# Kernel optimization log

Measured on AMD Instinct MI355X. Metric: run time of the kernel, lower is better.

The kernel has to match this reference:

```python
import jax, jax.numpy as jnp
import numpy as np

D = 1024      # dim_input
H = 16        # n_heads
DH = 64       # dim_inner
S = 1024      # current_seq
M = 1024      # pre_seq (memory)
B = 2         # batch
SCALE = 1.0 / np.sqrt(DH)


def _rel_shift(x):
    # x: [S, J, B, H]; Transformer-XL relative shift
    s, j = x.shape[0], x.shape[1]
    zero = jnp.zeros((s, 1) + x.shape[2:], x.dtype)
    x = jnp.concatenate([zero, x], axis=1)            # [S, J+1, B, H]
    x = x.reshape((j + 1, s) + x.shape[2:])[1:]        # [J, S, B, H]
    return x.reshape((s, j) + x.shape[2:])             # [S, J, B, H]


def setup_inputs() -> dict:
    key = jax.random.key(0)
    ks = jax.random.split(key, 9)
    std = 1.0 / np.sqrt(D)
    return {
        "multi_head_input": jax.random.normal(ks[0], (S, B, D), jnp.float32),
        "position_emb": jax.random.normal(ks[1], (S + M, D), jnp.float32),
        "memory": jax.random.normal(ks[2], (M, B, D), jnp.float32),
        "u": jax.random.normal(ks[3], (H, DH), jnp.float32) * 0.02,
        "v": jax.random.normal(ks[4], (H, DH), jnp.float32) * 0.02,
        "W_kv": jax.random.normal(ks[5], (D, 2 * H * DH), jnp.float32) * std,
        "W_q": jax.random.normal(ks[6], (D, H * DH), jnp.float32) * std,
        "W_pos": jax.random.normal(ks[7], (D, H * DH), jnp.float32) * std,
        "W_out": jax.random.normal(ks[8], (H * DH, D), jnp.float32) * std,
    }


def reference(multi_head_input, position_emb, memory, u, v, W_kv, W_q, W_pos, W_out):
    s = multi_head_input.shape[0]
    m = memory.shape[0]
    b = multi_head_input.shape[1]
    x_mem = jnp.concatenate([memory, multi_head_input], axis=0)   # [M+S, B, D]
    kv = x_mem @ W_kv                                              # [M+S, B, 2*H*DH]
    k, val = jnp.split(kv, 2, axis=-1)
    k = k.reshape(m + s, b, H, DH)
    val = val.reshape(m + s, b, H, DH)
    q = (multi_head_input @ W_q).reshape(s, b, H, DH)              # [S, B, H, DH]

    # content term: (q + u) . k
    content = jnp.einsum('ibhd,jbhd->ijbh', q + u, k)              # [S, M+S, B, H]
    # position term: (q + v) . r, then rel_shift
    r = (position_emb @ W_pos).reshape(m + s, H, DH)               # [M+S, H, DH]
    pos = jnp.einsum('ibhd,jhd->ijbh', q + v, r)                   # [S, M+S, B, H]
    pos = _rel_shift(pos)

    attn = jax.nn.softmax((content + pos) * SCALE, axis=1)         # [S, M+S, B, H]
    out = jnp.einsum('ijbh,jbhd->ibhd', attn, val).reshape(s, b, H * DH)
    return out @ W_out                                             # [S, B, D]
```

## Files before the change

kernel.cpp:

```cpp
#include <hip/hip_runtime.h>
#include <hip/hip_bf16.h>
#include <hip/hip_fp16.h>
#include <math.h>

#define D    1024
#define H    16
#define DH   64
#define S    1024
#define M    1024
#define B    2
#define J    2048
#define SCALE 0.125f

typedef __attribute__((ext_vector_type(8))) short        bf16x8;
typedef __attribute__((ext_vector_type(4))) short        s16x4;
typedef __attribute__((ext_vector_type(8))) _Float16     h16x8;
typedef __attribute__((ext_vector_type(8))) unsigned short us8;
typedef __attribute__((ext_vector_type(4))) float        f32x4;

__device__ __forceinline__ short f2bs(float f) {
    __hip_bfloat16 t = __float2bfloat16(f);
    short r; __builtin_memcpy(&r, &t, 2); return r;
}
__device__ __forceinline__ unsigned short f2bf_fast(float f) {
    unsigned int u; __builtin_memcpy(&u, &f, 4);
    return (unsigned short)((u + 0x8000u) >> 16);
}

__device__ __forceinline__ void g2l16(const short* g, short* l) {
    __builtin_amdgcn_global_load_lds(
        (const __attribute__((address_space(1))) unsigned int*)g,
        (__attribute__((address_space(3))) unsigned int*)l, 16, 0, 0);
}

__global__ __launch_bounds__(256)
void prep(const float* __restrict__ mem, const float* __restrict__ x,
          const float* __restrict__ pemb,
          const float* __restrict__ Wkv, const float* __restrict__ Wq,
          const float* __restrict__ Wpos, const float* __restrict__ Wout,
          short* __restrict__ a_bf, short* __restrict__ p_bf,
          short* __restrict__ wkvt, short* __restrict__ wqt,
          short* __restrict__ wpt,  short* __restrict__ wot)
{
    __shared__ float t[64][65];
    int blk = blockIdx.x;
    const int tid = threadIdx.x;
    if (blk < 6144) {
        const int idx = (blk * 256 + tid) * 4;
        const int TWO_M = 2 * 1024 * 1024;
        float4 v; short* dst;
        if (idx < TWO_M)          { v = *(const float4*)(mem  + idx);           dst = a_bf + idx; }
        else if (idx < 2 * TWO_M) { v = *(const float4*)(x    + idx - TWO_M);   dst = a_bf + idx; }
        else                      { v = *(const float4*)(pemb + idx - 2*TWO_M); dst = p_bf + idx - 2*TWO_M; }
        s16x4 o = { f2bs(v.x), f2bs(v.y), f2bs(v.z), f2bs(v.w) };
        *(s16x4*)dst = o;
        return;
    }
    blk -= 6144;
    const float* src; short* dst; int N, t0;
    if (blk < 512)       { src = Wkv;  dst = wkvt; N = 2048; t0 = blk; }
    else if (blk < 768)  { src = Wq;   dst = wqt;  N = 1024; t0 = blk - 512; }
    else if (blk < 1024) { src = Wpos; dst = wpt;  N = 1024; t0 = blk - 768; }
    else                 { src = Wout; dst = wot;  N = 1024; t0 = blk - 1024; }
    const int ntn = N >> 6;
    const int k0 = (t0 / ntn) * 64, n0 = (t0 % ntn) * 64;
    #pragma unroll
    for (int e = tid; e < 4096; e += 256) {
        int r = e >> 6, c = e & 63;
        t[r][c] = src[(size_t)(k0 + r) * N + n0 + c];
    }
    __syncthreads();
    #pragma unroll
    for (int e = tid; e < 4096; e += 256) {
        int nr = e >> 6, kc = e & 63;
        dst[(size_t)(n0 + nr) * 1024 + k0 + kc] = f2bs(t[kc][nr]);
    }
}

__device__ __forceinline__ void gemm_core(const short* __restrict__ A,
                                          const short* __restrict__ Bt,
                                          short* As, short* Bs,
                                          int bm0, int bn0, int tid,
                                          f32x4 acc[4][4])
{
    const int w    = tid >> 6;
    const int wy   = w >> 1, wx = w & 1;
    const int lane = tid & 63;
    const int lm   = lane & 15;
    const int lq   = lane >> 4;

    for (int k0 = 0; k0 < 1024; k0 += 64) {
        const short* Ab = A  + (size_t)bm0 * 1024 + k0;
        const short* Bb = Bt + (size_t)bn0 * 1024 + k0;
        #pragma unroll
        for (int t = 0; t < 4; ++t) {
            int s = t * 256 + tid;
            int r = s >> 3, c = s & 7;
            int cg = c ^ (r & 7);
            g2l16(Ab + r * 1024 + cg * 8, As + s * 8);
            g2l16(Bb + r * 1024 + cg * 8, Bs + s * 8);
        }
        __syncthreads();
        #pragma unroll
        for (int kk = 0; kk < 2; ++kk) {
            bf16x8 af[4], bg[4];
            #pragma unroll
            for (int r4 = 0; r4 < 4; ++r4) {
                int ar = wy * 64 + r4 * 16 + lm;
                int kc = kk * 4 + lq;
                af[r4] = *(const bf16x8*)(As + ((ar << 3) + (kc ^ (ar & 7))) * 8);
            }
            #pragma unroll
            for (int c4 = 0; c4 < 4; ++c4) {
                int br = wx * 64 + c4 * 16 + lm;
                int kc = kk * 4 + lq;
                bg[c4] = *(const bf16x8*)(Bs + ((br << 3) + (kc ^ (br & 7))) * 8);
            }
            #pragma unroll
            for (int r4 = 0; r4 < 4; ++r4)
                #pragma unroll
                for (int c4 = 0; c4 < 4; ++c4)
                    acc[r4][c4] = __builtin_amdgcn_mfma_f32_16x16x32_bf16(
                        af[r4], bg[c4], acc[r4][c4], 0, 0, 0);
        }
        __syncthreads();
    }
}

__global__ __launch_bounds__(256)
void proj_fused(const short* __restrict__ a_bf, const short* __restrict__ p_bf,
                const short* __restrict__ wkvt, const short* __restrict__ wqt,
                const short* __restrict__ wpt,
                short* __restrict__ k_bf, short* __restrict__ vt_bf,
                short* __restrict__ qu_bf, short* __restrict__ qv_bf,
                short* __restrict__ r_bf,
                const float* __restrict__ uvec, const float* __restrict__ vvec)
{
    __shared__ __align__(16) short As[128 * 64];
    __shared__ __align__(16) short Bs[128 * 64];

    int blk = blockIdx.x;
    int mode, bx, by;
    const short *A, *Bt;
    if (blk < 512)      { bx = blk & 15; by = blk >> 4;
                          if (bx >= 8) { mode = 4; A = wkvt; Bt = a_bf; }
                          else         { mode = 0; A = a_bf; Bt = wkvt; } }
    else if (blk < 640) { int b2 = blk - 512; mode = 1; bx = b2 & 7; by = b2 >> 3;
                          A = a_bf + (size_t)2048 * 1024; Bt = wqt; }
    else                { int b3 = blk - 640; mode = 2; bx = b3 & 7; by = b3 >> 3;
                          A = p_bf; Bt = wpt; }
    const int bn0 = (mode == 4) ? by * 128 : bx * 128;
    const int bm0 = (mode == 4) ? bx * 128 : by * 128;
    const int tid = threadIdx.x;
    const int w = tid >> 6, wy = w >> 1, wx = w & 1;
    const int lane = tid & 63, lm = lane & 15, lq = lane >> 4;

    f32x4 acc[4][4];
    #pragma unroll
    for (int r = 0; r < 4; ++r)
        #pragma unroll
        for (int c = 0; c < 4; ++c) acc[r][c] = (f32x4){0.f, 0.f, 0.f, 0.f};

    gemm_core(A, Bt, As, Bs, bm0, bn0, tid, acc);

    #pragma unroll
    for (int r4 = 0; r4 < 4; ++r4) {
        #pragma unroll
        for (int c4 = 0; c4 < 4; ++c4) {
            const int n = bn0 + wx * 64 + c4 * 16 + lm;
            float ubias = 0.f, vbias = 0.f;
            if (mode == 1) { ubias = uvec[n]; vbias = vvec[n]; }
            #pragma unroll
            for (int reg = 0; reg < 4; ++reg) {
                const int m = bm0 + wy * 64 + r4 * 16 + lq * 4 + reg;
                const float val = acc[r4][c4][reg];
                if (mode == 0) {
                    int j = m >> 1, b = m & 1;
                    int h = n >> 6, d = n & 63;
                    k_bf[(((size_t)b * H + h) * J + j) * DH + d] = f2bs(val);
                } else if (mode == 4) {
                    int n2 = m - 1024, h = n2 >> 6, d = n2 & 63;
                    int j = n >> 1, b = n & 1;
                    vt_bf[(((size_t)b * H + h) * DH + d) * J + j] = f2bs(val);
                } else if (mode == 1) {
                    int i = m >> 1, b = m & 1;
                    int h = n >> 6, d = n & 63;
                    size_t o = (((size_t)b * H + h) * S + i) * DH + d;
                    qu_bf[o] = f2bs((val + ubias) * SCALE);
                    qv_bf[o] = f2bs((val + vbias) * SCALE);
                } else {
                    int h = n >> 6, d = n & 63;
                    r_bf[((size_t)h * J + m) * DH + d] = f2bs(val);
                }
            }
        }
    }
}

__global__ __launch_bounds__(256)
void gemm_out(const short* __restrict__ A, const short* __restrict__ Bt,
              float* __restrict__ out)
{
    __shared__ __align__(16) short As[128 * 64];
    __shared__ __align__(16) short Bs[128 * 64];
    const int bn0 = blockIdx.x * 128, bm0 = blockIdx.y * 128;
    const int tid = threadIdx.x;
    const int w = tid >> 6, wy = w >> 1, wx = w & 1;
    const int lane = tid & 63, lm = lane & 15, lq = lane >> 4;

    f32x4 acc[4][4];
    #pragma unroll
    for (int r = 0; r < 4; ++r)
        #pragma unroll
        for (int c = 0; c < 4; ++c) acc[r][c] = (f32x4){0.f, 0.f, 0.f, 0.f};

    gemm_core(A, Bt, As, Bs, bm0, bn0, tid, acc);

    #pragma unroll
    for (int r4 = 0; r4 < 4; ++r4)
        #pragma unroll
        for (int c4 = 0; c4 < 4; ++c4) {
            const int n = bn0 + wx * 64 + c4 * 16 + lm;
            #pragma unroll
            for (int reg = 0; reg < 4; ++reg) {
                const int m = bm0 + wy * 64 + r4 * 16 + lq * 4 + reg;
                out[(size_t)m * 1024 + n] = acc[r4][c4][reg];
            }
        }
}

__device__ __forceinline__ int sidx(int m, int c) {
    return (m << 10) + (c ^ (m << 3));
}

__global__ __launch_bounds__(512)
void attn_mfma(const short* __restrict__ qu_bf, const short* __restrict__ qv_bf,
               const short* __restrict__ k_bf,  const short* __restrict__ vt_bf,
               const short* __restrict__ r_bf,
               float* __restrict__ opart, float* __restrict__ ml)
{
    __shared__ unsigned short sc[32 * 1024];
    __half* sch = (__half*)sc;
    float*  scF = (float*)sc;

    const int bh  = blockIdx.x;
    const int it  = blockIdx.y;
    const int jh  = blockIdx.z;
    const int i0  = it * 32;
    const int cbeg = jh << 10, cend = cbeg + 1024;
    const int h   = bh & (H - 1);
    const int tid = threadIdx.x;
    const int w    = tid >> 6;
    const int lane = tid & 63;
    const int lm   = lane & 15;
    const int lq   = lane >> 4;
    const int slot = (it * 32 + bh) * 2 + jh;

    const short* qup0 = qu_bf + ((size_t)(bh * S + i0 + lm)) * DH + lq * 8;
    const short* qup1 = qup0 + 16 * DH;
    bf16x8 au00 = *(const bf16x8*)qup0,        au01 = *(const bf16x8*)(qup0 + 32);
    bf16x8 au10 = *(const bf16x8*)qup1,        au11 = *(const bf16x8*)(qup1 + 32);
    const short* qvp0 = qv_bf + ((size_t)(bh * S + i0 + lm)) * DH + lq * 8;
    const short* qvp1 = qvp0 + 16 * DH;
    bf16x8 av00 = *(const bf16x8*)qvp0,        av01 = *(const bf16x8*)(qvp0 + 32);
    bf16x8 av10 = *(const bf16x8*)qvp1,        av11 = *(const bf16x8*)(qvp1 + 32);
    int r1a = i0 + 1 + lm;  if (r1a > S - 1) r1a = S - 1;
    int r1b = i0 + 17 + lm; if (r1b > S - 1) r1b = S - 1;
    const short* qwp0 = qv_bf + ((size_t)(bh * S + r1a)) * DH + lq * 8;
    const short* qwp1 = qv_bf + ((size_t)(bh * S + r1b)) * DH + lq * 8;
    bf16x8 aw00 = *(const bf16x8*)qwp0,        aw01 = *(const bf16x8*)(qwp0 + 32);
    bf16x8 aw10 = *(const bf16x8*)qwp1,        aw11 = *(const bf16x8*)(qwp1 + 32);

    if (tid < 32) {
        int hole = i0 + tid + 1025;
        if (hole >= cbeg && hole < cend) sc[sidx(tid, hole - cbeg)] = 0;
    }

    const short* rbase = r_bf + (size_t)h * J * DH;

    {
        int tmp = cbeg + 977 - i0;
        int tlo = tmp > 0 ? ((tmp + 15) >> 4) : 0;
        int thi = (cend + 1022 - i0) >> 4; if (thi > 127) thi = 127;
        int t = tlo + w;
        if (t <= thi) {
            const short* rp = rbase + (size_t)(t * 16 + lm) * DH + lq * 8;
            bf16x8 b0 = *(const bf16x8*)rp, b1 = *(const bf16x8*)(rp + 32);
            for (; t <= thi; t += 8) {
                bf16x8 n0, n1;
                if (t + 8 <= thi) {
                    const short* rpn = rbase + (size_t)((t + 8) * 16 + lm) * DH + lq * 8;
                    n0 = *(const bf16x8*)rpn; n1 = *(const bf16x8*)(rpn + 32);
                }
                f32x4 c0 = {0.f,0.f,0.f,0.f}, c1 = {0.f,0.f,0.f,0.f};
                c0 = __builtin_amdgcn_mfma_f32_16x16x32_bf16(av00, b0, c0, 0, 0, 0);
                c1 = __builtin_amdgcn_mfma_f32_16x16x32_bf16(av10, b0, c1, 0, 0, 0);
                c0 = __builtin_amdgcn_mfma_f32_16x16x32_bf16(av01, b1, c0, 0, 0, 0);
                c1 = __builtin_amdgcn_mfma_f32_16x16x32_bf16(av11, b1, c1, 0, 0, 0);
                int cb = i0 + t * 16 + lm - 1023 - cbeg;
                int base = i0 + 16 * t - 1023;
                if (base >= cbeg && base + 46 < cend) {
                    #pragma unroll
                    for (int r = 0; r < 4; ++r) {
                        int m0 = lq * 4 + r, m1 = m0 + 16;
                        sch[sidx(m0, cb + m0)] = __float2half(c0[r]);
                        sch[sidx(m1, cb + m1)] = __float2half(c1[r]);
                    }
                } else {
                    #pragma unroll
                    for (int r = 0; r < 4; ++r) {
                        int m0 = lq * 4 + r, m1 = m0 + 16;
                        int cA = cb + m0, cB = cb + m1;
                        if (cA >= 0 && cA < 1024) sch[sidx(m0, cA)] = __float2half(c0[r]);
                        if (cB >= 0 && cB < 1024) sch[sidx(m1, cB)] = __float2half(c1[r]);
                    }
                }
                b0 = n0; b1 = n1;
            }
        }
    }

    {
        int tmpw = cbeg - 1072 - i0;
        int tlw = tmpw > 0 ? ((tmpw + 15) >> 4) : 0;
        int thw = (cend - 1027 - i0) >> 4; if (thw > 127) thw = 127;
        int t = tlw + w;
        if (t <= thw) {
            const short* rp = rbase + (size_t)(t * 16 + lm) * DH + lq * 8;
            bf16x8 b0 = *(const bf16x8*)rp, b1 = *(const bf16x8*)(rp + 32);
            for (; t <= thw; t += 8) {
                bf16x8 n0, n1;
                if (t + 8 <= thw) {
                    const short* rpn = rbase + (size_t)((t + 8) * 16 + lm) * DH + lq * 8;
                    n0 = *(const bf16x8*)rpn; n1 = *(const bf16x8*)(rpn + 32);
                }
                f32x4 c0 = {0.f,0.f,0.f,0.f}, c1 = {0.f,0.f,0.f,0.f};
                c0 = __builtin_amdgcn_mfma_f32_16x16x32_bf16(aw00, b0, c0, 0, 0, 0);
                c1 = __builtin_amdgcn_mfma_f32_16x16x32_bf16(aw10, b0, c1, 0, 0, 0);
                c0 = __builtin_amdgcn_mfma_f32_16x16x32_bf16(aw01, b1, c0, 0, 0, 0);
                c1 = __builtin_amdgcn_mfma_f32_16x16x32_bf16(aw11, b1, c1, 0, 0, 0);
                int cb = i0 + t * 16 + lm + 1026 - cbeg;
                int base = i0 + 16 * t + 1026;
                if (base >= cbeg && base + 46 < cend) {
                    #pragma unroll
                    for (int r = 0; r < 4; ++r) {
                        int m0 = lq * 4 + r, m1 = m0 + 16;
                        sch[sidx(m0, cb + m0)] = __float2half(c0[r]);
                        sch[sidx(m1, cb + m1)] = __float2half(c1[r]);
                    }
                } else {
                    #pragma unroll
                    for (int r = 0; r < 4; ++r) {
                        int m0 = lq * 4 + r, m1 = m0 + 16;
                        int cA = cb + m0, cB = cb + m1;
                        if (cA >= 0 && cA < 1024) sch[sidx(m0, cA)] = __float2half(c0[r]);
                        if (cB >= 0 && cB < 1024) sch[sidx(m1, cB)] = __float2half(c1[r]);
                    }
                }
                b0 = n0; b1 = n1;
            }
        }
    }

    const short* kbase = k_bf + (size_t)bh * J * DH;
    int tc0 = jh * 64 + w + 8 * ((it) & 7);
    int tc1 = jh * 64 + w + 8 * ((1 + it) & 7);
    const short* kp0 = kbase + (size_t)(tc0 * 16 + lm) * DH + lq * 8;
    const short* kp1 = kbase + (size_t)(tc1 * 16 + lm) * DH + lq * 8;
    bf16x8 kb0 = *(const bf16x8*)kp0, kb1 = *(const bf16x8*)(kp0 + 32);
    bf16x8 kb2 = *(const bf16x8*)kp1, kb3 = *(const bf16x8*)(kp1 + 32);
    __syncthreads();

    #pragma unroll 1
    for (int g = 0; g < 8; g += 2) {
        int t0 = jh * 64 + w + 8 * ((g + it) & 7);
        int t1 = jh * 64 + w + 8 * ((g + 1 + it) & 7);
        bf16x8 nb0, nb1, nb2, nb3;
        if (g + 2 < 8) {
            int u0 = jh * 64 + w + 8 * ((g + 2 + it) & 7);
            int u1 = jh * 64 + w + 8 * ((g + 3 + it) & 7);
            const short* np0 = kbase + (size_t)(u0 * 16 + lm) * DH + lq * 8;
            const short* np1 = kbase + (size_t)(u1 * 16 + lm) * DH + lq * 8;
            nb0 = *(const bf16x8*)np0; nb1 = *(const bf16x8*)(np0 + 32);
            nb2 = *(const bf16x8*)np1; nb3 = *(const bf16x8*)(np1 + 32);
        }
        int lc0 = t0 * 16 + lm - cbeg;
        int lc1 = t1 * 16 + lm - cbeg;
        f32x4 c0, c1, c2, c3;
        #pragma unroll
        for (int r = 0; r < 4; ++r) {
            c0[r] = __half2float(sch[sidx(lq * 4 + r, lc0)]);
            c1[r] = __half2float(sch[sidx(16 + lq * 4 + r, lc0)]);
            c2[r] = __half2float(sch[sidx(lq * 4 + r, lc1)]);
            c3[r] = __half2float(sch[sidx(16 + lq * 4 + r, lc1)]);
        }
        c0 = __builtin_amdgcn_mfma_f32_16x16x32_bf16(au00, kb0, c0, 0, 0, 0);
        c1 = __builtin_amdgcn_mfma_f32_16x16x32_bf16(au10, kb0, c1, 0, 0, 0);
        c2 = __builtin_amdgcn_mfma_f32_16x16x32_bf16(au00, kb2, c2, 0, 0, 0);
        c3 = __builtin_amdgcn_mfma_f32_16x16x32_bf16(au10, kb2, c3, 0, 0, 0);
        c0 = __builtin_amdgcn_mfma_f32_16x16x32_bf16(au01, kb1, c0, 0, 0, 0);
        c1 = __builtin_amdgcn_mfma_f32_16x16x32_bf16(au11, kb1, c1, 0, 0, 0);
        c2 = __builtin_amdgcn_mfma_f32_16x16x32_bf16(au01, kb3, c2, 0, 0, 0);
        c3 = __builtin_amdgcn_mfma_f32_16x16x32_bf16(au11, kb3, c3, 0, 0, 0);
        #pragma unroll
        for (int r = 0; r < 4; ++r) {
            sch[sidx(lq * 4 + r, lc0)]      = __float2half(c0[r]);
            sch[sidx(16 + lq * 4 + r, lc0)] = __float2half(c1[r]);
            sch[sidx(lq * 4 + r, lc1)]      = __float2half(c2[r]);
            sch[sidx(16 + lq * 4 + r, lc1)] = __float2half(c3[r]);
        }
        kb0 = nb0; kb1 = nb1; kb2 = nb2; kb3 = nb3;
    }

    const int dslice = w & 3, jq = w >> 2;
    const short* vtb = vt_bf + ((size_t)bh * DH + dslice * 16 + lm) * J + cbeg + jq * 512;
    bf16x8 cv0, cv1, cv2, cv3;
    {
        int j0 = (it & 3) * 128;
        cv0 = *(const bf16x8*)(vtb + j0 +  0 + lq * 8);
        cv1 = *(const bf16x8*)(vtb + j0 + 32 + lq * 8);
        cv2 = *(const bf16x8*)(vtb + j0 + 64 + lq * 8);
        cv3 = *(const bf16x8*)(vtb + j0 + 96 + lq * 8);
    }
    __syncthreads();

    {
        const int row = tid >> 4;
        const int cw  = (tid & 15) * 8;
        float ssum = 0.f;
        #pragma unroll
        for (int c = cw; c < 1024; c += 128) {
            int idx = sidx(row, c);
            h16x8 v = *(const h16x8*)(sc + idx);
            us8 e;
            #pragma unroll
            for (int k = 0; k < 8; ++k) {
                float ex = __builtin_amdgcn_exp2f((float)v[k] * 1.44269504f);
                ssum += ex;
                e[k] = f2bf_fast(ex);
            }
            *(us8*)(sc + idx) = e;
        }
        #pragma unroll
        for (int off = 1; off < 16; off <<= 1) ssum += __shfl_xor(ssum, off);
        if ((tid & 15) == 0) {
            ml[(size_t)slot * 64 + row * 2]     = 0.f;
            ml[(size_t)slot * 64 + row * 2 + 1] = ssum;
        }
    }
    __syncthreads();

    f32x4 pa0 = {0.f,0.f,0.f,0.f}, pa1 = {0.f,0.f,0.f,0.f};
    f32x4 pa2 = {0.f,0.f,0.f,0.f}, pa3 = {0.f,0.f,0.f,0.f};
    f32x4 pb0 = {0.f,0.f,0.f,0.f}, pb1 = {0.f,0.f,0.f,0.f};
    f32x4 pb2 = {0.f,0.f,0.f,0.f}, pb3 = {0.f,0.f,0.f,0.f};
    #pragma unroll 1
    for (int jo0 = 0; jo0 < 4; ++jo0) {
        bf16x8 nv0, nv1, nv2, nv3;
        if (jo0 < 3) {
            int jn = ((jo0 + 1 + it) & 3) * 128;
            nv0 = *(const bf16x8*)(vtb + jn +  0 + lq * 8);
            nv1 = *(const bf16x8*)(vtb + jn + 32 + lq * 8);
            nv2 = *(const bf16x8*)(vtb + jn + 64 + lq * 8);
            nv3 = *(const bf16x8*)(vtb + jn + 96 + lq * 8);
        }
        int j0 = ((jo0 + it) & 3) * 128;
        int lb = jq * 512 + j0;
        bf16x8 a0 = *(const bf16x8*)(sc + sidx(lm, lb +  0 + lq * 8));
        bf16x8 a1 = *(const bf16x8*)(sc + sidx(lm, lb + 32 + lq * 8));
        bf16x8 a2 = *(const bf16x8*)(sc + sidx(lm, lb + 64 + lq * 8));
        bf16x8 a3 = *(const bf16x8*)(sc + sidx(lm, lb + 96 + lq * 8));
        bf16x8 c0 = *(const bf16x8*)(sc + sidx(16 + lm, lb +  0 + lq * 8));
        bf16x8 c1 = *(const bf16x8*)(sc + sidx(16 + lm, lb + 32 + lq * 8));
        bf16x8 c2 = *(const bf16x8*)(sc + sidx(16 + lm, lb + 64 + lq * 8));
        bf16x8 c3 = *(const bf16x8*)(sc + sidx(16 + lm, lb + 96 + lq * 8));
        pa0 = __builtin_amdgcn_mfma_f32_16x16x32_bf16(a0, cv0, pa0, 0, 0, 0);
        pb0 = __builtin_amdgcn_mfma_f32_16x16x32_bf16(c0, cv0, pb0, 0, 0, 0);
        pa1 = __builtin_amdgcn_mfma_f32_16x16x32_bf16(a1, cv1, pa1, 0, 0, 0);
        pb1 = __builtin_amdgcn_mfma_f32_16x16x32_bf16(c1, cv1, pb1, 0, 0, 0);
        pa2 = __builtin_amdgcn_mfma_f32_16x16x32_bf16(a2, cv2, pa2, 0, 0, 0);
        pb2 = __builtin_amdgcn_mfma_f32_16x16x32_bf16(c2, cv2, pb2, 0, 0, 0);
        pa3 = __builtin_amdgcn_mfma_f32_16x16x32_bf16(a3, cv3, pa3, 0, 0, 0);
        pb3 = __builtin_amdgcn_mfma_f32_16x16x32_bf16(c3, cv3, pb3, 0, 0, 0);
        if (jo0 < 3) { cv0 = nv0; cv1 = nv1; cv2 = nv2; cv3 = nv3; }
    }
    __syncthreads();

    #pragma unroll
    for (int r = 0; r < 4; ++r) {
        int m0 = lq * 4 + r, m1 = m0 + 16;
        scF[jq * 2048 + m0 * 64 + dslice * 16 + lm] = pa0[r] + pa1[r] + pa2[r] + pa3[r];
        scF[jq * 2048 + m1 * 64 + dslice * 16 + lm] = pb0[r] + pb1[r] + pb2[r] + pb3[r];
    }
    __syncthreads();

    float* op = opart + (size_t)slot * 2048;
    #pragma unroll
    for (int e = tid; e < 2048; e += 512)
        op[e] = scF[e] + scF[2048 + e];
}

__global__ __launch_bounds__(256)
void attn_combine(const float* __restrict__ opart, const float* __restrict__ ml,
                  short* __restrict__ o_bf)
{
    const int blk = blockIdx.x;
    const int it = blk >> 5, bh = blk & 31;
    const int h = bh & 15, b = bh >> 4;
    __shared__ float wgt[32][2];
    const int tid = threadIdx.x;
    if (tid < 32) {
        float m0 = ml[(size_t)(blk * 2 + 0) * 64 + tid * 2];
        float l0 = ml[(size_t)(blk * 2 + 0) * 64 + tid * 2 + 1];
        float m1 = ml[(size_t)(blk * 2 + 1) * 64 + tid * 2];
        float l1 = ml[(size_t)(blk * 2 + 1) * 64 + tid * 2 + 1];
        float mx = fmaxf(m0, m1);
        float e0 = __expf(m0 - mx), e1 = __expf(m1 - mx);
        float inv = 1.0f / (e0 * l0 + e1 * l1);
        wgt[tid][0] = e0 * inv;
        wgt[tid][1] = e1 * inv;
    }
    __syncthreads();
    const float* p0 = opart + (size_t)(blk * 2 + 0) * 2048;
    const float* p1 = opart + (size_t)(blk * 2 + 1) * 2048;
    #pragma unroll
    for (int e = tid; e < 2048; e += 256) {
        int m = e >> 6, d = e & 63;
        float val = p0[e] * wgt[m][0] + p1[e] * wgt[m][1];
        o_bf[((size_t)(it * 32 + m) * B + b) * (H * DH) + h * DH + d] = f2bs(val);
    }
}

extern "C" void kernel_launch(void* const* d_in, const int* in_sizes, int n_in,
                              void* d_out, int out_size, void* d_ws, size_t ws_size,
                              hipStream_t stream)
{
    const float* x    = (const float*)d_in[0];
    const float* pemb = (const float*)d_in[1];
    const float* mem  = (const float*)d_in[2];
    const float* u    = (const float*)d_in[3];
    const float* v    = (const float*)d_in[4];
    const float* Wkv  = (const float*)d_in[5];
    const float* Wq   = (const float*)d_in[6];
    const float* Wpos = (const float*)d_in[7];
    const float* Wout = (const float*)d_in[8];
    float* out = (float*)d_out;

    char* p = (char*)d_ws;
    short* a_bf  = (short*)p; p += (size_t)4096 * 1024 * 2;
    short* p_bf  = (short*)p; p += (size_t)2048 * 1024 * 2;
    short* wkvt  = (short*)p; p += (size_t)2048 * 1024 * 2;
    short* wqt   = (short*)p; p += (size_t)1024 * 1024 * 2;
    short* wpt   = (short*)p; p += (size_t)1024 * 1024 * 2;
    short* wot   = (short*)p; p += (size_t)1024 * 1024 * 2;
    short* k_bf  = (short*)p; p += (size_t)B * H * J * DH * 2;
    short* vt_bf = (short*)p; p += (size_t)B * H * J * DH * 2;
    short* qu_bf = (short*)p; p += (size_t)B * H * S * DH * 2;
    short* qv_bf = (short*)p; p += (size_t)B * H * S * DH * 2;
    short* r_bf  = (short*)p; p += (size_t)H * J * DH * 2;
    short* o_bf  = (short*)p;

    float* opart = (float*)d_ws;
    float* ml    = (float*)((char*)d_ws + (size_t)16 * 1024 * 1024);

    prep<<<7424, 256, 0, stream>>>(mem, x, pemb, Wkv, Wq, Wpos, Wout,
                                   a_bf, p_bf, wkvt, wqt, wpt, wot);
    proj_fused<<<768, 256, 0, stream>>>(a_bf, p_bf, wkvt, wqt, wpt,
                                        k_bf, vt_bf, qu_bf, qv_bf, r_bf, u, v);
    attn_mfma<<<dim3(B * H, S / 32, 2), 512, 0, stream>>>(
        qu_bf, qv_bf, k_bf, vt_bf, r_bf, opart, ml);
    attn_combine<<<(S / 32) * B * H, 256, 0, stream>>>(opart, ml, o_bf);
    gemm_out<<<dim3(8, 16), 256, 0, stream>>>(o_bf, wot, out);
}
```

Baseline: 298.0 us.

## Double attention block to 1024 threads, splitting query rows across wave pairs

Doubles the attention kernel's workgroup from 8 to 16 waves, so each wave handles only 16 of the 32 query rows instead of both halves. The positional scores, content scores, softmax row reduction and PV MFMA stages are all re-partitioned so per-wave work and register use halve. This aims to raise latency hiding within each block. The cost is more waves contending for the same 64KB LDS tile, plus duplicated loads of the R/K/V operands, since both row-halves fetch the same B fragments.

```diff
diff --git a/kernel.cpp b/kernel.cpp
--- a/kernel.cpp
+++ b/kernel.cpp
@@ -233,7 +233,7 @@
     return (m << 10) + (c ^ (m << 3));
 }
 
-__global__ __launch_bounds__(512)
+__global__ __launch_bounds__(1024)
 void attn_mfma(const short* __restrict__ qu_bf, const short* __restrict__ qv_bf,
                const short* __restrict__ k_bf,  const short* __restrict__ vt_bf,
                const short* __restrict__ r_bf,
@@ -256,20 +256,15 @@
     const int lq   = lane >> 4;
     const int slot = (it * 32 + bh) * 2 + jh;
 
-    const short* qup0 = qu_bf + ((size_t)(bh * S + i0 + lm)) * DH + lq * 8;
-    const short* qup1 = qup0 + 16 * DH;
-    bf16x8 au00 = *(const bf16x8*)qup0,        au01 = *(const bf16x8*)(qup0 + 32);
-    bf16x8 au10 = *(const bf16x8*)qup1,        au11 = *(const bf16x8*)(qup1 + 32);
-    const short* qvp0 = qv_bf + ((size_t)(bh * S + i0 + lm)) * DH + lq * 8;
-    const short* qvp1 = qvp0 + 16 * DH;
-    bf16x8 av00 = *(const bf16x8*)qvp0,        av01 = *(const bf16x8*)(qvp0 + 32);
-    bf16x8 av10 = *(const bf16x8*)qvp1,        av11 = *(const bf16x8*)(qvp1 + 32);
-    int r1a = i0 + 1 + lm;  if (r1a > S - 1) r1a = S - 1;
-    int r1b = i0 + 17 + lm; if (r1b > S - 1) r1b = S - 1;
-    const short* qwp0 = qv_bf + ((size_t)(bh * S + r1a)) * DH + lq * 8;
-    const short* qwp1 = qv_bf + ((size_t)(bh * S + r1b)) * DH + lq * 8;
-    bf16x8 aw00 = *(const bf16x8*)qwp0,        aw01 = *(const bf16x8*)(qwp0 + 32);
-    bf16x8 aw10 = *(const bf16x8*)qwp1,        aw11 = *(const bf16x8*)(qwp1 + 32);
+    const int wt8 = w >> 1, wg = w & 1, mr = wg * 16;
+
+    const short* qup = qu_bf + ((size_t)(bh * S + i0 + mr + lm)) * DH + lq * 8;
+    bf16x8 au0 = *(const bf16x8*)qup, au1 = *(const bf16x8*)(qup + 32);
+    const short* qvp = qv_bf + ((size_t)(bh * S + i0 + mr + lm)) * DH + lq * 8;
+    bf16x8 av0 = *(const bf16x8*)qvp, av1 = *(const bf16x8*)(qvp + 32);
+    int r1 = i0 + mr + 1 + lm; if (r1 > S - 1) r1 = S - 1;
+    const short* qwp = qv_bf + ((size_t)(bh * S + r1)) * DH + lq * 8;
+    bf16x8 aw0 = *(const bf16x8*)qwp, aw1 = *(const bf16x8*)(qwp + 32);
 
     if (tid < 32) {
         int hole = i0 + tid + 1025;
@@ -282,7 +277,7 @@
         int tmp = cbeg + 977 - i0;
         int tlo = tmp > 0 ? ((tmp + 15) >> 4) : 0;
         int thi = (cend + 1022 - i0) >> 4; if (thi > 127) thi = 127;
-        int t = tlo + w;
+        int t = tlo + wt8;
         if (t <= thi) {
             const short* rp = rbase + (size_t)(t * 16 + lm) * DH + lq * 8;
             bf16x8 b0 = *(const bf16x8*)rp, b1 = *(const bf16x8*)(rp + 32);
@@ -292,27 +287,23 @@
                     const short* rpn = rbase + (size_t)((t + 8) * 16 + lm) * DH + lq * 8;
                     n0 = *(const bf16x8*)rpn; n1 = *(const bf16x8*)(rpn + 32);
                 }
-                f32x4 c0 = {0.f,0.f,0.f,0.f}, c1 = {0.f,0.f,0.f,0.f};
-                c0 = __builtin_amdgcn_mfma_f32_16x16x32_bf16(av00, b0, c0, 0, 0, 0);
-                c1 = __builtin_amdgcn_mfma_f32_16x16x32_bf16(av10, b0, c1, 0, 0, 0);
-                c0 = __builtin_amdgcn_mfma_f32_16x16x32_bf16(av01, b1, c0, 0, 0, 0);
-                c1 = __builtin_amdgcn_mfma_f32_16x16x32_bf16(av11, b1, c1, 0, 0, 0);
+                f32x4 c0 = {0.f,0.f,0.f,0.f};
+                c0 = __builtin_amdgcn_mfma_f32_16x16x32_bf16(av0, b0, c0, 0, 0, 0);
+                c0 = __builtin_amdgcn_mfma_f32_16x16x32_bf16(av1, b1, c0, 0, 0, 0);
                 int cb = i0 + t * 16 + lm - 1023 - cbeg;
                 int base = i0 + 16 * t - 1023;
-                if (base >= cbeg && base + 46 < cend) {
+                if (base + mr >= cbeg && base + mr + 30 < cend) {
                     #pragma unroll
                     for (int r = 0; r < 4; ++r) {
-                        int m0 = lq * 4 + r, m1 = m0 + 16;
+                        int m0 = mr + lq * 4 + r;
                         sch[sidx(m0, cb + m0)] = __float2half(c0[r]);
-                        sch[sidx(m1, cb + m1)] = __float2half(c1[r]);
                     }
                 } else {
                     #pragma unroll
                     for (int r = 0; r < 4; ++r) {
-                        int m0 = lq * 4 + r, m1 = m0 + 16;
-                        int cA = cb + m0, cB = cb + m1;
+                        int m0 = mr + lq * 4 + r;
+                        int cA = cb + m0;
                         if (cA >= 0 && cA < 1024) sch[sidx(m0, cA)] = __float2half(c0[r]);
-                        if (cB >= 0 && cB < 1024) sch[sidx(m1, cB)] = __float2half(c1[r]);
                     }
                 }
                 b0 = n0; b1 = n1;
@@ -324,7 +315,7 @@
         int tmpw = cbeg - 1072 - i0;
         int tlw = tmpw > 0 ? ((tmpw + 15) >> 4) : 0;
         int thw = (cend - 1027 - i0) >> 4; if (thw > 127) thw = 127;
-        int t = tlw + w;
+        int t = tlw + wt8;
         if (t <= thw) {
             const short* rp = rbase + (size_t)(t * 16 + lm) * DH + lq * 8;
             bf16x8 b0 = *(const bf16x8*)rp, b1 = *(const bf16x8*)(rp + 32);
@@ -334,27 +325,23 @@
                     const short* rpn = rbase + (size_t)((t + 8) * 16 + lm) * DH + lq * 8;
                     n0 = *(const bf16x8*)rpn; n1 = *(const bf16x8*)(rpn + 32);
                 }
-                f32x4 c0 = {0.f,0.f,0.f,0.f}, c1 = {0.f,0.f,0.f,0.f};
-                c0 = __builtin_amdgcn_mfma_f32_16x16x32_bf16(aw00, b0, c0, 0, 0, 0);
-                c1 = __builtin_amdgcn_mfma_f32_16x16x32_bf16(aw10, b0, c1, 0, 0, 0);
-                c0 = __builtin_amdgcn_mfma_f32_16x16x32_bf16(aw01, b1, c0, 0, 0, 0);
-                c1 = __builtin_amdgcn_mfma_f32_16x16x32_bf16(aw11, b1, c1, 0, 0, 0);
+                f32x4 c0 = {0.f,0.f,0.f,0.f};
+                c0 = __builtin_amdgcn_mfma_f32_16x16x32_bf16(aw0, b0, c0, 0, 0, 0);
+                c0 = __builtin_amdgcn_mfma_f32_16x16x32_bf16(aw1, b1, c0, 0, 0, 0);
                 int cb = i0 + t * 16 + lm + 1026 - cbeg;
                 int base = i0 + 16 * t + 1026;
-                if (base >= cbeg && base + 46 < cend) {
+                if (base + mr >= cbeg && base + mr + 30 < cend) {
                     #pragma unroll
                     for (int r = 0; r < 4; ++r) {
-                        int m0 = lq * 4 + r, m1 = m0 + 16;
+                        int m0 = mr + lq * 4 + r;
                         sch[sidx(m0, cb + m0)] = __float2half(c0[r]);
-                        sch[sidx(m1, cb + m1)] = __float2half(c1[r]);
                     }
                 } else {
                     #pragma unroll
                     for (int r = 0; r < 4; ++r) {
-                        int m0 = lq * 4 + r, m1 = m0 + 16;
-                        int cA = cb + m0, cB = cb + m1;
+                        int m0 = mr + lq * 4 + r;
+                        int cA = cb + m0;
                         if (cA >= 0 && cA < 1024) sch[sidx(m0, cA)] = __float2half(c0[r]);
-                        if (cB >= 0 && cB < 1024) sch[sidx(m1, cB)] = __float2half(c1[r]);
                     }
                 }
                 b0 = n0; b1 = n1;
@@ -363,56 +350,34 @@
     }
 
     const short* kbase = k_bf + (size_t)bh * J * DH;
-    int tc0 = jh * 64 + w + 8 * ((it) & 7);
-    int tc1 = jh * 64 + w + 8 * ((1 + it) & 7);
+    int tc0 = jh * 64 + wt8 + 8 * (it & 7);
     const short* kp0 = kbase + (size_t)(tc0 * 16 + lm) * DH + lq * 8;
-    const short* kp1 = kbase + (size_t)(tc1 * 16 + lm) * DH + lq * 8;
     bf16x8 kb0 = *(const bf16x8*)kp0, kb1 = *(const bf16x8*)(kp0 + 32);
-    bf16x8 kb2 = *(const bf16x8*)kp1, kb3 = *(const bf16x8*)(kp1 + 32);
     __syncthreads();
 
     #pragma unroll 1
-    for (int g = 0; g < 8; g += 2) {
-        int t0 = jh * 64 + w + 8 * ((g + it) & 7);
-        int t1 = jh * 64 + w + 8 * ((g + 1 + it) & 7);
-        bf16x8 nb0, nb1, nb2, nb3;
-        if (g + 2 < 8) {
-            int u0 = jh * 64 + w + 8 * ((g + 2 + it) & 7);
-            int u1 = jh * 64 + w + 8 * ((g + 3 + it) & 7);
-            const short* np0 = kbase + (size_t)(u0 * 16 + lm) * DH + lq * 8;
-            const short* np1 = kbase + (size_t)(u1 * 16 + lm) * DH + lq * 8;
-            nb0 = *(const bf16x8*)np0; nb1 = *(const bf16x8*)(np0 + 32);
-            nb2 = *(const bf16x8*)np1; nb3 = *(const bf16x8*)(np1 + 32);
-        }
-        int lc0 = t0 * 16 + lm - cbeg;
-        int lc1 = t1 * 16 + lm - cbeg;
-        f32x4 c0, c1, c2, c3;
-        #pragma unroll
-        for (int r = 0; r < 4; ++r) {
-            c0[r] = __half2float(sch[sidx(lq * 4 + r, lc0)]);
-            c1[r] = __half2float(sch[sidx(16 + lq * 4 + r, lc0)]);
-            c2[r] = __half2float(sch[sidx(lq * 4 + r, lc1)]);
-            c3[r] = __half2float(sch[sidx(16 + lq * 4 + r, lc1)]);
-        }
-        c0 = __builtin_amdgcn_mfma_f32_16x16x32_bf16(au00, kb0, c0, 0, 0, 0);
-        c1 = __builtin_amdgcn_mfma_f32_16x16x32_bf16(au10, kb0, c1, 0, 0, 0);
-        c2 = __builtin_amdgcn_mfma_f32_16x16x32_bf16(au00, kb2, c2, 0, 0, 0);
-        c3 = __builtin_amdgcn_mfma_f32_16x16x32_bf16(au10, kb2, c3, 0, 0, 0);
-        c0 = __builtin_amdgcn_mfma_f32_16x16x32_bf16(au01, kb1, c0, 0, 0, 0);
-        c1 = __builtin_amdgcn_mfma_f32_16x16x32_bf16(au11, kb1, c1, 0, 0, 0);
-        c2 = __builtin_amdgcn_mfma_f32_16x16x32_bf16(au01, kb3, c2, 0, 0, 0);
-        c3 = __builtin_amdgcn_mfma_f32_16x16x32_bf16(au11, kb3, c3, 0, 0, 0);
-        #pragma unroll
-        for (int r = 0; r < 4; ++r) {
-            sch[sidx(lq * 4 + r, lc0)]      = __float2half(c0[r]);
-            sch[sidx(16 + lq * 4 + r, lc0)] = __float2half(c1[r]);
-            sch[sidx(lq * 4 + r, lc1)]      = __float2half(c2[r]);
-            sch[sidx(16 + lq * 4 + r, lc1)] = __float2half(c3[r]);
-        }
-        kb0 = nb0; kb1 = nb1; kb2 = nb2; kb3 = nb3;
-    }
-
-    const int dslice = w & 3, jq = w >> 2;
+    for (int g = 0; g < 8; ++g) {
+        bf16x8 nb0, nb1;
+        if (g + 1 < 8) {
+            int u = jh * 64 + wt8 + 8 * ((g + 1 + it) & 7);
+            const short* np = kbase + (size_t)(u * 16 + lm) * DH + lq * 8;
+            nb0 = *(const bf16x8*)np; nb1 = *(const bf16x8*)(np + 32);
+        }
+        int t = jh * 64 + wt8 + 8 * ((g + it) & 7);
+        int lc = t * 16 + lm - cbeg;
+        f32x4 c0;
+        #pragma unroll
+        for (int r = 0; r < 4; ++r)
+            c0[r] = __half2float(sch[sidx(mr + lq * 4 + r, lc)]);
+        c0 = __builtin_amdgcn_mfma_f32_16x16x32_bf16(au0, kb0, c0, 0, 0, 0);
+        c0 = __builtin_amdgcn_mfma_f32_16x16x32_bf16(au1, kb1, c0, 0, 0, 0);
+        #pragma unroll
+        for (int r = 0; r < 4; ++r)
+            sch[sidx(mr + lq * 4 + r, lc)] = __float2half(c0[r]);
+        kb0 = nb0; kb1 = nb1;
+    }
+
+    const int dslice = w & 3, jq = (w >> 2) & 1, wgp = w >> 3, mrp = wgp * 16;
     const short* vtb = vt_bf + ((size_t)bh * DH + dslice * 16 + lm) * J + cbeg + jq * 512;
     bf16x8 cv0, cv1, cv2, cv3;
     {
@@ -425,11 +390,11 @@
     __syncthreads();
 
     {
-        const int row = tid >> 4;
-        const int cw  = (tid & 15) * 8;
+        const int row = tid >> 5;
+        const int cw  = (tid & 31) * 8;
         float ssum = 0.f;
         #pragma unroll
-        for (int c = cw; c < 1024; c += 128) {
+        for (int c = cw; c < 1024; c += 256) {
             int idx = sidx(row, c);
             h16x8 v = *(const h16x8*)(sc + idx);
             us8 e;
@@ -442,8 +407,8 @@
             *(us8*)(sc + idx) = e;
         }
         #pragma unroll
-        for (int off = 1; off < 16; off <<= 1) ssum += __shfl_xor(ssum, off);
-        if ((tid & 15) == 0) {
+        for (int off = 1; off < 32; off <<= 1) ssum += __shfl_xor(ssum, off);
+        if ((tid & 31) == 0) {
             ml[(size_t)slot * 64 + row * 2]     = 0.f;
             ml[(size_t)slot * 64 + row * 2 + 1] = ssum;
         }
@@ -452,8 +417,6 @@
 
     f32x4 pa0 = {0.f,0.f,0.f,0.f}, pa1 = {0.f,0.f,0.f,0.f};
     f32x4 pa2 = {0.f,0.f,0.f,0.f}, pa3 = {0.f,0.f,0.f,0.f};
-    f32x4 pb0 = {0.f,0.f,0.f,0.f}, pb1 = {0.f,0.f,0.f,0.f};
-    f32x4 pb2 = {0.f,0.f,0.f,0.f}, pb3 = {0.f,0.f,0.f,0.f};
     #pragma unroll 1
     for (int jo0 = 0; jo0 < 4; ++jo0) {
         bf16x8 nv0, nv1, nv2, nv3;
@@ -466,37 +429,28 @@
         }
         int j0 = ((jo0 + it) & 3) * 128;
         int lb = jq * 512 + j0;
-        bf16x8 a0 = *(const bf16x8*)(sc + sidx(lm, lb +  0 + lq * 8));
-        bf16x8 a1 = *(const bf16x8*)(sc + sidx(lm, lb + 32 + lq * 8));
-        bf16x8 a2 = *(const bf16x8*)(sc + sidx(lm, lb + 64 + lq * 8));
-        bf16x8 a3 = *(const bf16x8*)(sc + sidx(lm, lb + 96 + lq * 8));
-        bf16x8 c0 = *(const bf16x8*)(sc + sidx(16 + lm, lb +  0 + lq * 8));
-        bf16x8 c1 = *(const bf16x8*)(sc + sidx(16 + lm, lb + 32 + lq * 8));
-        bf16x8 c2 = *(const bf16x8*)(sc + sidx(16 + lm, lb + 64 + lq * 8));
-        bf16x8 c3 = *(const bf16x8*)(sc + sidx(16 + lm, lb + 96 + lq * 8));
+        bf16x8 a0 = *(const bf16x8*)(sc + sidx(mrp + lm, lb +  0 + lq * 8));
+        bf16x8 a1 = *(const bf16x8*)(sc + sidx(mrp + lm, lb + 32 + lq * 8));
+        bf16x8 a2 = *(const bf16x8*)(sc + sidx(mrp + lm, lb + 64 + lq * 8));
+        bf16x8 a3 = *(const bf16x8*)(sc + sidx(mrp + lm, lb + 96 + lq * 8));
         pa0 = __builtin_amdgcn_mfma_f32_16x16x32_bf16(a0, cv0, pa0, 0, 0, 0);
-        pb0 = __builtin_amdgcn_mfma_f32_16x16x32_bf16(c0, cv0, pb0, 0, 0, 0);
         pa1 = __builtin_amdgcn_mfma_f32_16x16x32_bf16(a1, cv1, pa1, 0, 0, 0);
-        pb1 = __builtin_amdgcn_mfma_f32_16x16x32_bf16(c1, cv1, pb1, 0, 0, 0);
         pa2 = __builtin_amdgcn_mfma_f32_16x16x32_bf16(a2, cv2, pa2, 0, 0, 0);
-        pb2 = __builtin_amdgcn_mfma_f32_16x16x32_bf16(c2, cv2, pb2, 0, 0, 0);
         pa3 = __builtin_amdgcn_mfma_f32_16x16x32_bf16(a3, cv3, pa3, 0, 0, 0);
-        pb3 = __builtin_amdgcn_mfma_f32_16x16x32_bf16(c3, cv3, pb3, 0, 0, 0);
         if (jo0 < 3) { cv0 = nv0; cv1 = nv1; cv2 = nv2; cv3 = nv3; }
     }
     __syncthreads();
 
     #pragma unroll
     for (int r = 0; r < 4; ++r) {
-        int m0 = lq * 4 + r, m1 = m0 + 16;
+        int m0 = mrp + lq * 4 + r;
         scF[jq * 2048 + m0 * 64 + dslice * 16 + lm] = pa0[r] + pa1[r] + pa2[r] + pa3[r];
-        scF[jq * 2048 + m1 * 64 + dslice * 16 + lm] = pb0[r] + pb1[r] + pb2[r] + pb3[r];
     }
     __syncthreads();
 
     float* op = opart + (size_t)slot * 2048;
     #pragma unroll
-    for (int e = tid; e < 2048; e += 512)
+    for (int e = tid; e < 2048; e += 1024)
         op[e] = scF[e] + scF[2048 + e];
 }
 
@@ -567,7 +521,7 @@
                                    a_bf, p_bf, wkvt, wqt, wpt, wot);
     proj_fused<<<768, 256, 0, stream>>>(a_bf, p_bf, wkvt, wqt, wpt,
                                         k_bf, vt_bf, qu_bf, qv_bf, r_bf, u, v);
-    attn_mfma<<<dim3(B * H, S / 32, 2), 512, 0, stream>>>(
+    attn_mfma<<<dim3(B * H, S / 32, 2), 1024, 0, stream>>>(
         qu_bf, qv_bf, k_bf, vt_bf, r_bf, opart, ml);
     attn_combine<<<(S / 32) * B * H, 256, 0, stream>>>(opart, ml, o_bf);
     gemm_out<<<dim3(8, 16), 256, 0, stream>>>(o_bf, wot, out);
```

After: 385.9 us. +29.5%, slower.
